# Performance work log

Hardware: AMD Instinct MI355X
Metric: run time of the kernel (lower is better)

The kernel has to match this reference:

```python
import jax, jax.numpy as jnp
import numpy as np

EPS = 1e-8


def setup_inputs() -> dict:
    key = jax.random.key(0)
    k1, k2 = jax.random.split(key)
    B, C, L = 16, 4, 4096
    K, S = 256, 128
    x = jax.random.normal(k1, (B, C, L), dtype=jnp.float32)
    shapelets = jax.random.normal(k2, (C, K, S), dtype=jnp.float32)
    return {"x": x, "shapelets": shapelets}


def reference(x, shapelets):
    # x: (B, C, L); shapelets: (C, K, S)
    B, C, L = x.shape
    _, K, S = shapelets.shape
    W = L - S + 1  # number of sliding windows

    # unfold: (B, C, W, S) sliding windows with stride 1
    idx = jnp.arange(W)[:, None] + jnp.arange(S)[None, :]  # (W, S)
    win = x[:, :, idx]  # (B, C, W, S)
    win = win / jnp.maximum(jnp.linalg.norm(win, axis=-1, keepdims=True), EPS)

    shp = shapelets / jnp.maximum(
        jnp.linalg.norm(shapelets, axis=-1, keepdims=True), EPS
    )  # (C, K, S)

    # pairwise dot products: (B, C, W, K)
    sim = jnp.einsum("bcws,cks->bcwk", win, shp)
    # sum over channels, keepdim, transpose(2,3), divide by n_dims
    sim = jnp.sum(sim, axis=1, keepdims=True) / C  # (B, 1, W, K)
    sim = jnp.transpose(sim, (0, 1, 3, 2))  # (B, 1, K, W)
    sim = jax.nn.relu(sim)
    # global max-pool over window positions -> (B, 1, K)
    return jnp.max(sim, axis=3)
```

## Files before the change

### kernel.cpp

```cpp
#include <hip/hip_runtime.h>
#include <hip/hip_bf16.h>

#define NB 16
#define NC 4
#define NL 4096
#define NK 256
#define NS 128
#define NW (NL - NS + 1)
#define WPB 512
#define KPB 128
#define XEL 640
#define XROW 656
#define EPSF 1e-8f

typedef __attribute__((ext_vector_type(8))) _Float16 f16x8;
typedef __attribute__((ext_vector_type(2))) _Float16 f16x2;
typedef __attribute__((ext_vector_type(4))) float floatx4;

typedef __attribute__((address_space(3))) unsigned int* lds_ptr_t;
typedef const __attribute__((address_space(1))) unsigned int* gbl_ptr_t;

__device__ inline short f2h(float f) {
    _Float16 h = (_Float16)f;
    short s;
    __builtin_memcpy(&s, &h, sizeof(short));
    return s;
}

__device__ inline void gload_lds16(const void* g, void* l) {
    __builtin_amdgcn_global_load_lds((gbl_ptr_t)g, (lds_ptr_t)l, 16, 0, 0);
}

__global__ __launch_bounds__(64)
void norm_shp_kernel(const float* __restrict__ shp, short* __restrict__ shpn) {
    int ck = blockIdx.x;
    int k = ck & (NK - 1);
    int lane = threadIdx.x;
    const float* p = shp + (size_t)ck * NS;
    float v0 = p[lane];
    float v1 = p[lane + 64];
    float ss = v0 * v0 + v1 * v1;
    #pragma unroll
    for (int o = 32; o > 0; o >>= 1) ss += __shfl_xor(ss, o, 64);
    float rn = 1.f / fmaxf(sqrtf(ss), EPSF);
    int s0 = lane, s1 = lane + 64;
    int d0 = ((((s0 >> 3) ^ (k & 15)) << 3) | (s0 & 7));
    int d1 = ((((s1 >> 3) ^ (k & 15)) << 3) | (s1 & 7));
    shpn[(size_t)ck * NS + d0] = f2h(v0 * rn);
    shpn[(size_t)ck * NS + d1] = f2h(v1 * rn);
}

__global__ __launch_bounds__(512, 1)
void mcs_main_kernel(const float* __restrict__ x,
                     const short* __restrict__ shpn,
                     float* __restrict__ out) {
    __shared__ f16x8 bs[NC][KPB * 16];
    __shared__ alignas(16) short xcp[NC][4][XROW];
    __shared__ union {
        float scratch[NC][XEL];
        struct { float invw[NC][WPB]; float epi[8][64]; } c;
    } u;

    const int kq = blockIdx.x, slot = blockIdx.y;
    const int b = slot >> 3, wslot = slot & 7;
    const int w0 = wslot * WPB;
    const int tid = threadIdx.x;
    const int lane = tid & 63, wv = tid >> 6;
    const int m = lane & 15, q = lane >> 4, r = m & 3;
    const int kh = wv & 1, wh = wv >> 1;

    float xv[NC], xv2[NC];
    {
        const int g0 = w0 + tid;
        #pragma unroll
        for (int c = 0; c < NC; c++)
            xv[c] = (g0 < NL) ? x[((size_t)b * NC + c) * NL + g0] : 0.f;
        if (tid < XEL - 512) {
            const int g1 = g0 + 512;
            #pragma unroll
            for (int c = 0; c < NC; c++)
                xv2[c] = (g1 < NL) ? x[((size_t)b * NC + c) * NL + g1] : 0.f;
        }
    }

    {
        const char* gbase = (const char*)shpn + (size_t)(kq * KPB) * NS * 2;
        #pragma unroll
        for (int c = 0; c < NC; c++) {
            const char* gc = gbase + (size_t)c * NK * NS * 2;
            char* lc = (char*)&bs[c][0];
            #pragma unroll
            for (int i = 0; i < 4; i++) {
                int off = (wv * 4 + i) * 1024;
                gload_lds16(gc + off + lane * 16, lc + off);
            }
        }
    }

    #pragma unroll
    for (int c = 0; c < NC; c++) {
        short hv = f2h(xv[c]);
        #pragma unroll
        for (int rr = 0; rr < 4; rr++) {
            int o2 = tid - rr;
            if (o2 >= 0) xcp[c][rr][o2] = hv;
        }
        u.scratch[c][tid] = xv[c] * xv[c];
        if (tid < XEL - 512) {
            short hv2 = f2h(xv2[c]);
            #pragma unroll
            for (int rr = 0; rr < 4; rr++)
                xcp[c][rr][tid + 512 - rr] = hv2;
            u.scratch[c][tid + 512] = xv2[c] * xv2[c];
        }
    }
    __syncthreads();

    if (wv < 4) {
        const int c = wv;
        const int base = lane * 10;
        float v[10];
        #pragma unroll
        for (int i = 0; i < 10; i++) v[i] = u.scratch[c][base + i];
        #pragma unroll
        for (int i = 1; i < 10; i++) v[i] += v[i - 1];
        float tt = v[9];
        #pragma unroll
        for (int o = 1; o < 64; o <<= 1) {
            float uu = __shfl_up(tt, o, 64);
            if (lane >= o) tt += uu;
        }
        float excl = tt - v[9];
        #pragma unroll
        for (int i = 0; i < 10; i++) u.scratch[c][base + i] = v[i] + excl;
    }
    __syncthreads();

    float ivreg[4];
    #pragma unroll
    for (int i = 0; i < 4; i++) {
        int ii = tid + 512 * i;
        int c = ii >> 9, o = ii & 511;
        float nn = u.scratch[c][o + 127] - (o ? u.scratch[c][o - 1] : 0.f);
        int w = w0 + o;
        ivreg[i] = (w < NW) ? 1.f / fmaxf(sqrtf(fmaxf(nn, 0.f)), EPSF) : 0.f;
    }
    __syncthreads();
    #pragma unroll
    for (int i = 0; i < 4; i++) {
        int ii = tid + 512 * i;
        u.c.invw[ii >> 9][ii & 511] = ivreg[i];
    }
    asm volatile("s_waitcnt vmcnt(0)" ::: "memory");
    __syncthreads();

    floatx4 tot[8][4];
    #pragma unroll
    for (int mt = 0; mt < 8; mt++)
        #pragma unroll
        for (int kt = 0; kt < 4; kt++)
            tot[mt][kt] = (floatx4){0.f, 0.f, 0.f, 0.f};

    #pragma unroll
    for (int c = 0; c < NC; c++) {
        f16x2 iv2[8];
        #pragma unroll
        for (int mt = 0; mt < 8; mt++) {
            _Float16 ih = (_Float16)u.c.invw[c][wh * 128 + mt * 16 + m];
            iv2[mt] = (f16x2){ih, ih};
        }
        #pragma unroll
        for (int s0 = 0; s0 < NS; s0 += 32) {
            f16x8 a[8];
            #pragma unroll
            for (int mt = 0; mt < 8; mt++) {
                int ts = wh * 128 + mt * 16 + m + s0 + q * 8;
                const uint2* pp = (const uint2*)&xcp[c][r][ts - r];
                union { uint2 uu[2]; f16x8 v; f16x2 h2[4]; } cv;
                cv.uu[0] = pp[0]; cv.uu[1] = pp[1];
                #pragma unroll
                for (int p2 = 0; p2 < 4; p2++) cv.h2[p2] *= iv2[mt];
                a[mt] = cv.v;
            }
            int cc = (s0 >> 3) + q;
            #pragma unroll
            for (int kt = 0; kt < 4; kt++) {
                int k = kh * 64 + kt * 16 + m;
                f16x8 bf = bs[c][(k << 4) | (cc ^ m)];
                #pragma unroll
                for (int mt = 0; mt < 8; mt++)
                    tot[mt][kt] = __builtin_amdgcn_mfma_f32_16x16x32_f16(
                        a[mt], bf, tot[mt][kt], 0, 0, 0);
            }
        }
    }

    #pragma unroll
    for (int kt = 0; kt < 4; kt++) {
        float mx = -1e30f;
        #pragma unroll
        for (int mt = 0; mt < 8; mt++) {
            floatx4 v = tot[mt][kt];
            mx = fmaxf(mx, fmaxf(fmaxf(v.x, v.y), fmaxf(v.z, v.w)));
        }
        mx = fmaxf(mx, __shfl_xor(mx, 16, 64));
        mx = fmaxf(mx, __shfl_xor(mx, 32, 64));
        if (lane < 16) u.c.epi[wv][kt * 16 + lane] = mx;
    }
    __syncthreads();
    if (tid < 128) {
        int kh_ = tid >> 6, j = tid & 63;
        float v = fmaxf(fmaxf(u.c.epi[kh_][j],     u.c.epi[kh_ + 2][j]),
                        fmaxf(u.c.epi[kh_ + 4][j], u.c.epi[kh_ + 6][j]));
        v = fmaxf(v, 0.f) * 0.25f;
        atomicMax((int*)out + (size_t)b * NK + kq * KPB + tid,
                  __float_as_int(v));
    }
}

extern "C" void kernel_launch(void* const* d_in, const int* in_sizes, int n_in,
                              void* d_out, int out_size, void* d_ws, size_t ws_size,
                              hipStream_t stream) {
    (void)in_sizes; (void)n_in; (void)out_size; (void)ws_size;
    const float* x   = (const float*)d_in[0];
    const float* shp = (const float*)d_in[1];
    float* out = (float*)d_out;

    short* shpn = (short*)d_ws;

    norm_shp_kernel<<<NC * NK, 64, 0, stream>>>(shp, shpn);
    mcs_main_kernel<<<dim3(2, 128), 512, 0, stream>>>(x, shpn, out);
}
```

Baseline: 71.11 us.

## Fuse shapelet normalization into main kernel, dropping the separate prep launch

```diff
diff --git a/kernel.cpp b/kernel.cpp
--- a/kernel.cpp
+++ b/kernel.cpp
@@ -17,9 +17,6 @@
 typedef __attribute__((ext_vector_type(2))) _Float16 f16x2;
 typedef __attribute__((ext_vector_type(4))) float floatx4;
 
-typedef __attribute__((address_space(3))) unsigned int* lds_ptr_t;
-typedef const __attribute__((address_space(1))) unsigned int* gbl_ptr_t;
-
 __device__ inline short f2h(float f) {
     _Float16 h = (_Float16)f;
     short s;
@@ -27,33 +24,10 @@
     return s;
 }
 
-__device__ inline void gload_lds16(const void* g, void* l) {
-    __builtin_amdgcn_global_load_lds((gbl_ptr_t)g, (lds_ptr_t)l, 16, 0, 0);
-}
-
-__global__ __launch_bounds__(64)
-void norm_shp_kernel(const float* __restrict__ shp, short* __restrict__ shpn) {
-    int ck = blockIdx.x;
-    int k = ck & (NK - 1);
-    int lane = threadIdx.x;
-    const float* p = shp + (size_t)ck * NS;
-    float v0 = p[lane];
-    float v1 = p[lane + 64];
-    float ss = v0 * v0 + v1 * v1;
-    #pragma unroll
-    for (int o = 32; o > 0; o >>= 1) ss += __shfl_xor(ss, o, 64);
-    float rn = 1.f / fmaxf(sqrtf(ss), EPSF);
-    int s0 = lane, s1 = lane + 64;
-    int d0 = ((((s0 >> 3) ^ (k & 15)) << 3) | (s0 & 7));
-    int d1 = ((((s1 >> 3) ^ (k & 15)) << 3) | (s1 & 7));
-    shpn[(size_t)ck * NS + d0] = f2h(v0 * rn);
-    shpn[(size_t)ck * NS + d1] = f2h(v1 * rn);
-}
-
 __global__ __launch_bounds__(512, 1)
-void mcs_main_kernel(const float* __restrict__ x,
-                     const short* __restrict__ shpn,
-                     float* __restrict__ out) {
+void mcs_kernel(const float* __restrict__ x,
+                const float* __restrict__ shp,
+                float* __restrict__ out) {
     __shared__ f16x8 bs[NC][KPB * 16];
     __shared__ alignas(16) short xcp[NC][4][XROW];
     __shared__ union {
@@ -83,19 +57,23 @@
         }
     }
 
+    const float* brow =
+        shp + ((size_t)(tid >> 7) * NK + (size_t)kq * KPB + (tid & 127)) * NS;
+    float bss = 0.f;
     {
-        const char* gbase = (const char*)shpn + (size_t)(kq * KPB) * NS * 2;
-        #pragma unroll
-        for (int c = 0; c < NC; c++) {
-            const char* gc = gbase + (size_t)c * NK * NS * 2;
-            char* lc = (char*)&bs[c][0];
-            #pragma unroll
-            for (int i = 0; i < 4; i++) {
-                int off = (wv * 4 + i) * 1024;
-                gload_lds16(gc + off + lane * 16, lc + off);
-            }
-        }
-    }
+        const float4* bp = (const float4*)brow;
+        #pragma unroll
+        for (int it = 0; it < 4; it++) {
+            float4 ch[8];
+            #pragma unroll
+            for (int j = 0; j < 8; j++) ch[j] = bp[it * 8 + j];
+            #pragma unroll
+            for (int j = 0; j < 8; j++)
+                bss += ch[j].x * ch[j].x + ch[j].y * ch[j].y
+                     + ch[j].z * ch[j].z + ch[j].w * ch[j].w;
+        }
+    }
+    const float brn = 1.f / fmaxf(sqrtf(bss), EPSF);
 
     #pragma unroll
     for (int c = 0; c < NC; c++) {
@@ -133,6 +111,28 @@
         float excl = tt - v[9];
         #pragma unroll
         for (int i = 0; i < 10; i++) u.scratch[c][base + i] = v[i] + excl;
+    }
+
+    {
+        const float4* bp = (const float4*)brow;
+        const int bc = tid >> 7, bk = tid & 127;
+        #pragma unroll
+        for (int it = 0; it < 4; it++) {
+            float4 ch[8];
+            #pragma unroll
+            for (int j = 0; j < 8; j++) ch[j] = bp[it * 8 + j];
+            #pragma unroll
+            for (int uu = 0; uu < 4; uu++) {
+                float4 c0 = ch[uu * 2], c1 = ch[uu * 2 + 1];
+                f16x8 w;
+                w[0] = (_Float16)(c0.x * brn); w[1] = (_Float16)(c0.y * brn);
+                w[2] = (_Float16)(c0.z * brn); w[3] = (_Float16)(c0.w * brn);
+                w[4] = (_Float16)(c1.x * brn); w[5] = (_Float16)(c1.y * brn);
+                w[6] = (_Float16)(c1.z * brn); w[7] = (_Float16)(c1.w * brn);
+                int unit = it * 4 + uu;
+                bs[bc][(bk << 4) | (unit ^ (bk & 15))] = w;
+            }
+        }
     }
     __syncthreads();
 
@@ -151,7 +151,6 @@
         int ii = tid + 512 * i;
         u.c.invw[ii >> 9][ii & 511] = ivreg[i];
     }
-    asm volatile("s_waitcnt vmcnt(0)" ::: "memory");
     __syncthreads();
 
     floatx4 tot[8][4];
@@ -221,13 +220,10 @@
 extern "C" void kernel_launch(void* const* d_in, const int* in_sizes, int n_in,
                               void* d_out, int out_size, void* d_ws, size_t ws_size,
                               hipStream_t stream) {
-    (void)in_sizes; (void)n_in; (void)out_size; (void)ws_size;
+    (void)in_sizes; (void)n_in; (void)out_size; (void)d_ws; (void)ws_size;
     const float* x   = (const float*)d_in[0];
     const float* shp = (const float*)d_in[1];
     float* out = (float*)d_out;
 
-    short* shpn = (short*)d_ws;
-
-    norm_shp_kernel<<<NC * NK, 64, 0, stream>>>(shp, shpn);
-    mcs_main_kernel<<<dim3(2, 128), 512, 0, stream>>>(x, shpn, out);
+    mcs_kernel<<<dim3(2, 128), 512, 0, stream>>>(x, shp, out);
 }
```

Result: slower. 80.85 us (+13.7%).
